# Optimization experiments

Measured on AMD Instinct MI355X. Metric: run time of the kernel, lower is better.

Reference implementation:

```python
import jax, jax.numpy as jnp
import numpy as np


def setup_inputs() -> dict:
    key = jax.random.key(0)
    ks = jax.random.split(key, 9)
    B, C, H, W = 4, 256, 64, 64
    Ci = C // 2
    s = 0.05  # keep activations numerically tame
    return {
        "x": jax.random.normal(ks[0], (B, C, H, W), jnp.float32),
        "w_g": jax.random.normal(ks[1], (Ci, C), jnp.float32) * s,
        "b_g": jax.random.normal(ks[2], (Ci,), jnp.float32) * s,
        "w_theta": jax.random.normal(ks[3], (Ci, C), jnp.float32) * s,
        "b_theta": jax.random.normal(ks[4], (Ci,), jnp.float32) * s,
        "w_phi": jax.random.normal(ks[5], (Ci, C), jnp.float32) * s,
        "b_phi": jax.random.normal(ks[6], (Ci,), jnp.float32) * s,
        "w_out": jax.random.normal(ks[7], (C, Ci), jnp.float32) * s,
        "b_out": jax.random.normal(ks[8], (C,), jnp.float32) * s,
    }


def reference(x, w_g, b_g, w_theta, b_theta, w_phi, b_phi, w_out, b_out):
    B, C, H, W = x.shape
    Ci = w_g.shape[0]
    N = H * W
    xr = x.reshape(B, C, N)  # flatten spatial dims

    def proj(w, b):  # 1x1 conv == per-pixel GEMM
        return jnp.einsum("oc,bcn->bon", w, xr) + b[None, :, None]

    g_x = proj(w_g, b_g)          # [B, Ci, N]
    theta_x = proj(w_theta, b_theta)
    phi_x = proj(w_phi, b_phi)

    scale = jnp.asarray(Ci, x.dtype) ** 0.5
    f = jnp.einsum("bci,bcj->bij", theta_x, phi_x) / scale  # [B, N, N]
    attn = jax.nn.softmax(f, axis=-1)

    # out[b,c,i] = sum_j g_x[b,c,j] * attn[b,i,j]
    out = jnp.einsum("bcj,bij->bci", g_x, attn)             # [B, Ci, N]
    y = jnp.einsum("oc,bcn->bon", w_out, out) + b_out[None, :, None]
    return y.reshape(B, C, H, W) + x
```

## Files before the change

kernel.cpp:

```cpp
#include <hip/hip_runtime.h>
#include <hip/hip_bf16.h>


typedef float f32x4 __attribute__((ext_vector_type(4)));
typedef float f32x16 __attribute__((ext_vector_type(16)));
typedef short s16x8 __attribute__((ext_vector_type(8)));
typedef short s16x4 __attribute__((ext_vector_type(4)));

#define B_  4
#define C_  256
#define CI_ 128
#define N_  4096

#define OFF_Q    (8ull  << 20)
#define OFF_K    (12ull << 20)
#define OFF_G    (16ull << 20)
#define OFF_WQK  (24ull << 20)
#define OFF_WG   (OFF_WQK + 131072)
#define OFF_WOUT (OFF_WG  + 65536)
#define OFF_BQK  (OFF_WOUT + 65536)
#define OFF_BG   (OFF_BQK + 1024)
#define OFF_BOUT (OFF_BG  + 512)
#define OFF_END  (OFF_BOUT + 1024)

__device__ inline f32x4 mfma16(s16x8 a, s16x8 b, f32x4 c) {
    return __builtin_amdgcn_mfma_f32_16x16x32_bf16(a, b, c, 0, 0, 0);
}
__device__ inline f32x16 mfma32(s16x8 a, s16x8 b, f32x16 c) {
    return __builtin_amdgcn_mfma_f32_32x32x16_bf16(a, b, c, 0, 0, 0);
}
__device__ inline s16x8 ld8(const __hip_bfloat16* p) { return *(const s16x8*)p; }
__device__ inline float b2f(short u) {
    return __uint_as_float(((unsigned int)(unsigned short)u) << 16);
}
__device__ inline unsigned int pk2(float a, float b) {
    __hip_bfloat162 h;
    h.x = __float2bfloat16(a); h.y = __float2bfloat16(b);
    return *(unsigned int*)&h;
}
__device__ inline void gload_lds16(const void* g, void* l) {
    __builtin_amdgcn_global_load_lds(
        (const __attribute__((address_space(1))) unsigned int*)g,
        (__attribute__((address_space(3))) unsigned int*)l, 16, 0, 0);
}
__device__ inline float fexp2(float x) { return __builtin_amdgcn_exp2f(x); }

__global__ void prep_weights(const float* wg, const float* bg,
                             const float* wt, const float* bt,
                             const float* wp, const float* bp,
                             const float* wo, const float* bo, char* ws) {
    __hip_bfloat16* Wqk  = (__hip_bfloat16*)(ws + OFF_WQK);
    __hip_bfloat16* Wg   = (__hip_bfloat16*)(ws + OFF_WG);
    __hip_bfloat16* Wout = (__hip_bfloat16*)(ws + OFF_WOUT);
    float* Bqk  = (float*)(ws + OFF_BQK);
    float* Bg   = (float*)(ws + OFF_BG);
    float* Bout = (float*)(ws + OFF_BOUT);
    const float rs = 0.08838834764831845f * 1.4426950408889634f;
    int idx = blockIdx.x * 256 + threadIdx.x;
    if (idx < 65536) {
        int r = idx >> 8, c = idx & 255;
        float v = (r < 128) ? wt[r * 256 + c] * rs : wp[(r - 128) * 256 + c];
        Wqk[idx] = __float2bfloat16(v);
    }
    if (idx < 32768) {
        Wg[idx]   = __float2bfloat16(wg[idx]);
        Wout[idx] = __float2bfloat16(wo[idx]);
    }
    if (idx < 256) { Bqk[idx] = (idx < 128) ? bt[idx] * rs : bp[idx - 128]; Bout[idx] = bo[idx]; }
    if (idx < 128) Bg[idx] = bg[idx];
}

__global__ __launch_bounds__(256) void proj(const float* x, char* ws) {
    const __hip_bfloat16* Wqk = (const __hip_bfloat16*)(ws + OFF_WQK);
    const __hip_bfloat16* Wg  = (const __hip_bfloat16*)(ws + OFF_WG);
    const float* Bqk = (const float*)(ws + OFF_BQK);
    const float* Bg  = (const float*)(ws + OFF_BG);
    __hip_bfloat16* Q  = (__hip_bfloat16*)(ws + OFF_Q);
    __hip_bfloat16* Kb = (__hip_bfloat16*)(ws + OFF_K);
    __hip_bfloat16* G  = (__hip_bfloat16*)(ws + OFF_G);

    __shared__ char at[32 * 512];

    int b = blockIdx.y, n0 = blockIdx.x * 32;
    int t = threadIdx.x;
    int w = t >> 6, l = t & 63, lr = l & 15, lg = l >> 4;

    {
        int n4 = (t & 7) * 4;
        int cp = t >> 3;
        const float* xb = x + ((size_t)b * C_) * N_ + n0 + n4;
#pragma unroll
        for (int p = 0; p < 4; p++) {
            int c0 = (p * 32 + cp) * 2;
            f32x4 vA = *(const f32x4*)(xb + (size_t)c0 * N_);
            f32x4 vB = *(const f32x4*)(xb + (size_t)(c0 + 1) * N_);
            int slot = c0 >> 3, coff = (c0 & 7) << 1;
#pragma unroll
            for (int i = 0; i < 4; i++) {
                int n = n4 + i;
                *(unsigned int*)(&at[n * 512 + ((slot ^ (n & 7)) << 4) + coff]) =
                    pk2(vA[i], vB[i]);
            }
        }
    }
    __syncthreads();

    f32x4 acc[4][2] = {};
    f32x4 accg[2][2] = {};
    int o0q = w * 64, o0g = w * 32;
#pragma unroll
    for (int kk = 0; kk < 8; kk++) {
        s16x8 a[2];
#pragma unroll
        for (int nf = 0; nf < 2; nf++) {
            int row = nf * 16 + lr;
            int s = (4 * kk + lg) ^ (row & 7);
            a[nf] = *(const s16x8*)(&at[row * 512 + s * 16]);
        }
#pragma unroll
        for (int of = 0; of < 4; of++) {
            s16x8 bb = ld8(Wqk + (size_t)(o0q + 16 * of + lr) * C_ + kk * 32 + lg * 8);
            acc[of][0] = mfma16(a[0], bb, acc[of][0]);
            acc[of][1] = mfma16(a[1], bb, acc[of][1]);
        }
#pragma unroll
        for (int og = 0; og < 2; og++) {
            s16x8 ag = ld8(Wg + (size_t)(o0g + 16 * og + lr) * C_ + kk * 32 + lg * 8);
            accg[og][0] = mfma16(ag, a[0], accg[og][0]);
            accg[og][1] = mfma16(ag, a[1], accg[og][1]);
        }
    }
#pragma unroll
    for (int of = 0; of < 4; of++) {
        int o = o0q + 16 * of + lr;
        float bias = Bqk[o];
#pragma unroll
        for (int nf = 0; nf < 2; nf++) {
#pragma unroll
            for (int i = 0; i < 4; i++) {
                int n = n0 + 16 * nf + lg * 4 + i;
                float v = acc[of][nf][i] + bias;
                if (o < 128) Q [(size_t)(b * N_ + n) * CI_ + o]         = __float2bfloat16(v);
                else         Kb[(size_t)(b * N_ + n) * CI_ + (o - 128)] = __float2bfloat16(v);
            }
        }
    }
#pragma unroll
    for (int og = 0; og < 2; og++) {
#pragma unroll
        for (int i = 0; i < 4; i++) {
            int o = o0g + 16 * og + lg * 4 + i;
            float bias = Bg[o];
#pragma unroll
            for (int nf = 0; nf < 2; nf++) {
                int n = n0 + 16 * nf + lr;
                G[(size_t)(b * CI_ + o) * N_ + n] = __float2bfloat16(accg[og][nf][i] + bias);
            }
        }
    }
}

__global__ __launch_bounds__(256, 3) void flash9(char* ws, int nchunk,
                                                 unsigned long long off_part,
                                                 unsigned long long off_ml) {
    const __hip_bfloat16* Q  = (const __hip_bfloat16*)(ws + OFF_Q);
    const __hip_bfloat16* Kb = (const __hip_bfloat16*)(ws + OFF_K);
    const __hip_bfloat16* G  = (const __hip_bfloat16*)(ws + OFF_G);
    __hip_bfloat16* OP = (__hip_bfloat16*)(ws + off_part);
    float* ML = (float*)(ws + off_ml);

    __shared__ char kbuf[2][32 * 256];
    __shared__ char vbuf[2][128 * 64];

    int L = blockIdx.x;
    int npairs = B_ * nchunk;
    int pair = L % npairs, qt = L / npairs;
    int b = pair / nchunk, cz = pair % nchunk;
    int per = 128 / nchunk, rem = 128 % nchunk;
    int jb_t = per * cz + (cz < rem ? cz : rem);
    int sz_t = per + (cz < rem ? 1 : 0);
    int jb = jb_t << 5, je = jb + (sz_t << 5);

    int w = threadIdx.x >> 6, l = threadIdx.x & 63;
    int cl = l & 31, hi = l >> 5;
    int q0 = qt * 128 + w * 32;
    int kkey = (l & 7) << 4;
    int vkey = (l >> 1) & 3;

    auto STAGE = [&](int pb_, int j0_) {
#pragma unroll
        for (int i = 0; i < 2; i++) {
            int row = w * 8 + i * 4 + (l >> 4);
            int bcol = ((l & 15) << 4) ^ ((row & 7) << 4);
            const char* src = (const char*)Kb + (((size_t)b * N_ + j0_ + row) << 8) + bcol;
            gload_lds16(src, &kbuf[pb_][(w * 8 + i * 4) * 256]);
        }
#pragma unroll
        for (int i = 0; i < 2; i++) {
            int c = w * 32 + i * 16 + (l >> 2);
            int srcslot = (l & 3) ^ ((l >> 3) & 3);
            const char* src = (const char*)G + ((((size_t)b * CI_ + c) * N_ + j0_) << 1)
                              + (srcslot << 4);
            gload_lds16(src, &vbuf[pb_][(w * 32 + i * 16) * 64]);
        }
    };

    s16x8 qb[8];
    {
        const __hip_bfloat16* qrow = Q + ((size_t)b * N_ + q0 + cl) * CI_ + hi * 8;
#pragma unroll
        for (int st = 0; st < 8; st++) qb[st] = ld8(qrow + st * 16);
    }

    f32x16 oacc[4] = {};
    float m_i = 0.f, lsum = 0.f;

    STAGE(0, jb);
    __syncthreads();
    int pb = 0;

    for (int j0 = jb; j0 < je; j0 += 32) {
        if (j0 + 32 < je) STAGE(pb ^ 1, j0 + 32);
        const char* kb = kbuf[pb];
        const char* vbb = vbuf[pb];
        f32x16 s = {};
        __builtin_amdgcn_s_setprio(1);
#pragma unroll
        for (int st = 0; st < 8; st++) {
            s16x8 kf = *(const s16x8*)(kb + cl * 256 + ((((st << 1) + hi) << 4) ^ kkey));
            s = mfma32(kf, qb[st], s);
        }
        __builtin_amdgcn_s_setprio(0);
        if (j0 == jb) {
            float t0 = fmaxf(fmaxf(s[0], s[1]), fmaxf(s[2], s[3]));
            float t1 = fmaxf(fmaxf(s[4], s[5]), fmaxf(s[6], s[7]));
            float t2 = fmaxf(fmaxf(s[8], s[9]), fmaxf(s[10], s[11]));
            float t3 = fmaxf(fmaxf(s[12], s[13]), fmaxf(s[14], s[15]));
            float tm = fmaxf(fmaxf(t0, t1), fmaxf(t2, t3));
            tm = fmaxf(tm, __shfl_xor(tm, 32));
            m_i = tm;
        }
#pragma unroll
        for (int r = 0; r < 16; r++) s[r] = fexp2(s[r] - m_i);
        lsum += ((s[0] + s[1]) + (s[2] + s[3])) + ((s[4] + s[5]) + (s[6] + s[7]))
              + ((s[8] + s[9]) + (s[10] + s[11])) + ((s[12] + s[13]) + (s[14] + s[15]));
        union { unsigned int u[4]; s16x8 v; } pa0, pa1;
#pragma unroll
        for (int i = 0; i < 4; i++) {
            pa0.u[i] = pk2(s[2 * i], s[2 * i + 1]);
            pa1.u[i] = pk2(s[8 + 2 * i], s[9 + 2 * i]);
        }
        __builtin_amdgcn_s_setprio(1);
#pragma unroll
        for (int u = 0; u < 2; u++) {
            s16x8 pa = u ? pa1.v : pa0.v;
#pragma unroll
            for (int cb = 0; cb < 4; cb++) {
                const char* base = vbb + ((cb * 32 + cl) << 6) + hi * 8;
                union { s16x4 h[2]; s16x8 v; } vf;
                vf.h[0] = *(const s16x4*)(base + ((((u << 1))     ^ vkey) << 4));
                vf.h[1] = *(const s16x4*)(base + ((((u << 1) | 1) ^ vkey) << 4));
                oacc[cb] = mfma32(pa, vf.v, oacc[cb]);
            }
        }
        __builtin_amdgcn_s_setprio(0);
        __syncthreads();
        pb ^= 1;
    }
    lsum += __shfl_xor(lsum, 32);
#pragma unroll
    for (int cb = 0; cb < 4; cb++) {
#pragma unroll
        for (int r = 0; r < 16; r++) {
            int q = q0 + (r & 3) + 8 * (r >> 2) + 4 * hi;
            OP[((size_t)(cz * B_ + b) * N_ + q) * CI_ + cb * 32 + cl] =
                __float2bfloat16(oacc[cb][r]);
        }
    }
    if (l < 32) {
        size_t mi = ((size_t)(cz * B_ + b) * N_ + q0 + l) * 2;
        ML[mi] = m_i;
        ML[mi + 1] = lsum;
    }
}

template <int NC>
__global__ __launch_bounds__(256) void out_fused2(const float* x, char* ws, float* y,
                                                  unsigned long long off_part,
                                                  unsigned long long off_ml) {
    const __hip_bfloat16* OP = (const __hip_bfloat16*)(ws + off_part);
    const float* ML = (const float*)(ws + off_ml);
    const __hip_bfloat16* Wo = (const __hip_bfloat16*)(ws + OFF_WOUT);
    const float* Bout = (const float*)(ws + OFF_BOUT);

    __shared__ char oT[16 * 256];

    int b = blockIdx.y;
    int n0 = blockIdx.x * 16;
    int t = threadIdx.x;

    {
        int nl = t >> 4;
        int cg = t & 15;
        int n = n0 + nl;
        float mz[NC], lz[NC], M = -1e30f;
#pragma unroll
        for (int z = 0; z < NC; z++) {
            size_t mi = ((size_t)(z * B_ + b) * N_ + n) * 2;
            mz[z] = ML[mi]; lz[z] = ML[mi + 1];
            M = fmaxf(M, mz[z]);
        }
        float Ls = 0.f, wz[NC];
#pragma unroll
        for (int z = 0; z < NC; z++) { wz[z] = fexp2(mz[z] - M); Ls += lz[z] * wz[z]; }
        float inv = 1.f / Ls;
        float o8[8] = {};
#pragma unroll
        for (int z = 0; z < NC; z++) {
            s16x8 v = ld8(OP + ((size_t)(z * B_ + b) * N_ + n) * CI_ + cg * 8);
            float wv = wz[z] * inv;
#pragma unroll
            for (int e = 0; e < 8; e++) o8[e] += wv * b2f(v[e]);
        }
        union { unsigned int u[4]; s16x8 v; } r;
#pragma unroll
        for (int e = 0; e < 4; e++) r.u[e] = pk2(o8[2 * e], o8[2 * e + 1]);
        *(s16x8*)(&oT[nl * 256 + ((cg ^ (nl & 7)) << 4)]) = r.v;
    }
    __syncthreads();

    int w = t >> 6, l = t & 63, lr = l & 15, lg = l >> 4;
    int o0 = w * 64;
    f32x4 acc[4] = {};
#pragma unroll
    for (int kk = 0; kk < 4; kk++) {
        int slot = kk * 4 + lg;
        s16x8 bb = *(const s16x8*)(&oT[lr * 256 + ((slot ^ (lr & 7)) << 4)]);
#pragma unroll
        for (int of = 0; of < 4; of++) {
            s16x8 a = ld8(Wo + (size_t)(o0 + 16 * of + lr) * CI_ + kk * 32 + lg * 8);
            acc[of] = mfma16(a, bb, acc[of]);
        }
    }
#pragma unroll
    for (int of = 0; of < 4; of++) {
#pragma unroll
        for (int i = 0; i < 4; i++) {
            int o = o0 + 16 * of + lg * 4 + i;
            int n = n0 + lr;
            size_t idx = (size_t)(b * C_ + o) * N_ + n;
            y[idx] = acc[of][i] + Bout[o] + x[idx];
        }
    }
}

extern "C" void kernel_launch(void* const* d_in, const int* in_sizes, int n_in,
                              void* d_out, int out_size, void* d_ws, size_t ws_size,
                              hipStream_t stream) {
    const float* x  = (const float*)d_in[0];
    const float* wg = (const float*)d_in[1];
    const float* bg = (const float*)d_in[2];
    const float* wt = (const float*)d_in[3];
    const float* bt = (const float*)d_in[4];
    const float* wp = (const float*)d_in[5];
    const float* bp = (const float*)d_in[6];
    const float* wo = (const float*)d_in[7];
    const float* bo = (const float*)d_in[8];
    char* ws = (char*)d_ws;
    float* y = (float*)d_out;

    unsigned long long need6 = OFF_END + (24ull << 20) + (1ull << 20);
    unsigned long long need4 = OFF_END + (16ull << 20) + (1ull << 20);
    int nchunk;
    unsigned long long off_part, off_ml;
    if (ws_size >= need6) {
        nchunk = 6; off_part = OFF_END; off_ml = OFF_END + (24ull << 20);
    } else if (ws_size >= need4) {
        nchunk = 4; off_part = OFF_END; off_ml = OFF_END + (16ull << 20);
    } else {
        nchunk = 2; off_part = 0ull; off_ml = OFF_END;
    }

    prep_weights<<<256, 256, 0, stream>>>(wg, bg, wt, bt, wp, bp, wo, bo, ws);
    proj<<<dim3(128, 4), 256, 0, stream>>>(x, ws);
    flash9<<<dim3(32 * B_ * nchunk), 256, 0, stream>>>(ws, nchunk, off_part, off_ml);
    if (nchunk == 6)
        out_fused2<6><<<dim3(256, 4), 256, 0, stream>>>(x, ws, y, off_part, off_ml);
    else if (nchunk == 4)
        out_fused2<4><<<dim3(256, 4), 256, 0, stream>>>(x, ws, y, off_part, off_ml);
    else
        out_fused2<2><<<dim3(256, 4), 256, 0, stream>>>(x, ws, y, off_part, off_ml);
}
```

Baseline: 95.92 us.

## Rewrite flash attention kernel with 16x16 MFMA tiles and LDS-staged P

The attention kernel moves from 32x32x16 MFMAs with 128-query blocks to 16x16x32 MFMAs with 64-query blocks, where each wave handles 16 queries. P is re-laid out through a small per-wave LDS buffer before the PV product. Occupancy is raised to 4 blocks per CU and the 6-chunk key split is dropped in favour of at most 4 chunks. More blocks and higher occupancy trade against twice the K/V staging per query and the extra LDS round-trip for P.

```diff
diff --git a/kernel.cpp b/kernel.cpp
--- a/kernel.cpp
+++ b/kernel.cpp
@@ -3,9 +3,7 @@
 
 
 typedef float f32x4 __attribute__((ext_vector_type(4)));
-typedef float f32x16 __attribute__((ext_vector_type(16)));
 typedef short s16x8 __attribute__((ext_vector_type(8)));
-typedef short s16x4 __attribute__((ext_vector_type(4)));
 
 #define B_  4
 #define C_  256
@@ -25,9 +23,6 @@
 
 __device__ inline f32x4 mfma16(s16x8 a, s16x8 b, f32x4 c) {
     return __builtin_amdgcn_mfma_f32_16x16x32_bf16(a, b, c, 0, 0, 0);
-}
-__device__ inline f32x16 mfma32(s16x8 a, s16x8 b, f32x16 c) {
-    return __builtin_amdgcn_mfma_f32_32x32x16_bf16(a, b, c, 0, 0, 0);
 }
 __device__ inline s16x8 ld8(const __hip_bfloat16* p) { return *(const s16x8*)p; }
 __device__ inline float b2f(short u) {
@@ -160,9 +155,9 @@
     }
 }
 
-__global__ __launch_bounds__(256, 3) void flash9(char* ws, int nchunk,
-                                                 unsigned long long off_part,
-                                                 unsigned long long off_ml) {
+__global__ __launch_bounds__(256, 4) void flash16(char* ws, int nchunk,
+                                                  unsigned long long off_part,
+                                                  unsigned long long off_ml) {
     const __hip_bfloat16* Q  = (const __hip_bfloat16*)(ws + OFF_Q);
     const __hip_bfloat16* Kb = (const __hip_bfloat16*)(ws + OFF_K);
     const __hip_bfloat16* G  = (const __hip_bfloat16*)(ws + OFF_G);
@@ -171,21 +166,20 @@
 
     __shared__ char kbuf[2][32 * 256];
     __shared__ char vbuf[2][128 * 64];
+    __shared__ char pbuf[4][1024];
 
     int L = blockIdx.x;
     int npairs = B_ * nchunk;
     int pair = L % npairs, qt = L / npairs;
     int b = pair / nchunk, cz = pair % nchunk;
-    int per = 128 / nchunk, rem = 128 % nchunk;
-    int jb_t = per * cz + (cz < rem ? cz : rem);
-    int sz_t = per + (cz < rem ? 1 : 0);
-    int jb = jb_t << 5, je = jb + (sz_t << 5);
-
-    int w = threadIdx.x >> 6, l = threadIdx.x & 63;
-    int cl = l & 31, hi = l >> 5;
-    int q0 = qt * 128 + w * 32;
-    int kkey = (l & 7) << 4;
-    int vkey = (l >> 1) & 3;
+    int CH = N_ / nchunk;
+    int jb = cz * CH, je = jb + CH;
+
+    int w = threadIdx.x >> 6, l = threadIdx.x & 63, lr = l & 15, lg = l >> 4;
+    int q0 = qt * 64 + w * 16;
+    int swz  = (lr & 7) << 4;
+    int pswz = ((lr >> 1) & 3) << 4;
+    char* pw = &pbuf[w][0];
 
     auto STAGE = [&](int pb_, int j0_) {
 #pragma unroll
@@ -205,14 +199,14 @@
         }
     };
 
-    s16x8 qb[8];
+    s16x8 qa[4];
     {
-        const __hip_bfloat16* qrow = Q + ((size_t)b * N_ + q0 + cl) * CI_ + hi * 8;
-#pragma unroll
-        for (int st = 0; st < 8; st++) qb[st] = ld8(qrow + st * 16);
-    }
-
-    f32x16 oacc[4] = {};
+        const __hip_bfloat16* qrow = Q + ((size_t)b * N_ + q0 + lr) * CI_ + lg * 8;
+#pragma unroll
+        for (int kk = 0; kk < 4; kk++) qa[kk] = ld8(qrow + kk * 32);
+    }
+
+    f32x4 oacc[8] = {};
     float m_i = 0.f, lsum = 0.f;
 
     STAGE(0, jb);
@@ -223,62 +217,69 @@
         if (j0 + 32 < je) STAGE(pb ^ 1, j0 + 32);
         const char* kb = kbuf[pb];
         const char* vbb = vbuf[pb];
-        f32x16 s = {};
+        f32x4 s[2] = {};
         __builtin_amdgcn_s_setprio(1);
 #pragma unroll
-        for (int st = 0; st < 8; st++) {
-            s16x8 kf = *(const s16x8*)(kb + cl * 256 + ((((st << 1) + hi) << 4) ^ kkey));
-            s = mfma32(kf, qb[st], s);
+        for (int kk = 0; kk < 4; kk++) {
+            int bc = ((kk << 6) + (lg << 4)) ^ swz;
+            s16x8 kf0 = *(const s16x8*)(kb + lr * 256 + bc);
+            s16x8 kf1 = *(const s16x8*)(kb + (16 + lr) * 256 + bc);
+            s[0] = mfma16(kf0, qa[kk], s[0]);
+            s[1] = mfma16(kf1, qa[kk], s[1]);
         }
         __builtin_amdgcn_s_setprio(0);
         if (j0 == jb) {
-            float t0 = fmaxf(fmaxf(s[0], s[1]), fmaxf(s[2], s[3]));
-            float t1 = fmaxf(fmaxf(s[4], s[5]), fmaxf(s[6], s[7]));
-            float t2 = fmaxf(fmaxf(s[8], s[9]), fmaxf(s[10], s[11]));
-            float t3 = fmaxf(fmaxf(s[12], s[13]), fmaxf(s[14], s[15]));
-            float tm = fmaxf(fmaxf(t0, t1), fmaxf(t2, t3));
+            f32x4 m4;
+            m4[0] = fmaxf(s[0][0], s[1][0]); m4[1] = fmaxf(s[0][1], s[1][1]);
+            m4[2] = fmaxf(s[0][2], s[1][2]); m4[3] = fmaxf(s[0][3], s[1][3]);
+            float tm = fmaxf(fmaxf(m4[0], m4[1]), fmaxf(m4[2], m4[3]));
+            tm = fmaxf(tm, __shfl_xor(tm, 16));
             tm = fmaxf(tm, __shfl_xor(tm, 32));
             m_i = tm;
         }
-#pragma unroll
-        for (int r = 0; r < 16; r++) s[r] = fexp2(s[r] - m_i);
-        lsum += ((s[0] + s[1]) + (s[2] + s[3])) + ((s[4] + s[5]) + (s[6] + s[7]))
-              + ((s[8] + s[9]) + (s[10] + s[11])) + ((s[12] + s[13]) + (s[14] + s[15]));
-        union { unsigned int u[4]; s16x8 v; } pa0, pa1;
-#pragma unroll
-        for (int i = 0; i < 4; i++) {
-            pa0.u[i] = pk2(s[2 * i], s[2 * i + 1]);
-            pa1.u[i] = pk2(s[8 + 2 * i], s[9 + 2 * i]);
-        }
+        {
+            f32x4 sum4 = {};
+#pragma unroll
+            for (int t = 0; t < 2; t++) {
+#pragma unroll
+                for (int i = 0; i < 4; i++) s[t][i] = fexp2(s[t][i] - m_i);
+                sum4 += s[t];
+            }
+            lsum += (sum4[0] + sum4[1]) + (sum4[2] + sum4[3]);
+            char* base = pw + lr * 64;
+#pragma unroll
+            for (int t = 0; t < 2; t++) {
+                unsigned int lo = pk2(s[t][0], s[t][1]);
+                unsigned int hi = pk2(s[t][2], s[t][3]);
+                int slot = t * 2 + (lg >> 1);
+                int byte0 = ((slot << 4) ^ pswz) + ((lg & 1) << 3);
+                *(unsigned int*)(base + byte0)     = lo;
+                *(unsigned int*)(base + byte0 + 4) = hi;
+            }
+        }
+        s16x8 pa = *(const s16x8*)(pw + lr * 64 + ((lg << 4) ^ pswz));
         __builtin_amdgcn_s_setprio(1);
 #pragma unroll
-        for (int u = 0; u < 2; u++) {
-            s16x8 pa = u ? pa1.v : pa0.v;
-#pragma unroll
-            for (int cb = 0; cb < 4; cb++) {
-                const char* base = vbb + ((cb * 32 + cl) << 6) + hi * 8;
-                union { s16x4 h[2]; s16x8 v; } vf;
-                vf.h[0] = *(const s16x4*)(base + ((((u << 1))     ^ vkey) << 4));
-                vf.h[1] = *(const s16x4*)(base + ((((u << 1) | 1) ^ vkey) << 4));
-                oacc[cb] = mfma32(pa, vf.v, oacc[cb]);
-            }
+        for (int cf = 0; cf < 8; cf++) {
+            s16x8 vb = *(const s16x8*)(vbb + ((16 * cf + lr) << 6) +
+                                       ((lg << 4) ^ pswz));
+            oacc[cf] = mfma16(pa, vb, oacc[cf]);
         }
         __builtin_amdgcn_s_setprio(0);
         __syncthreads();
         pb ^= 1;
     }
+    lsum += __shfl_xor(lsum, 16);
     lsum += __shfl_xor(lsum, 32);
 #pragma unroll
-    for (int cb = 0; cb < 4; cb++) {
-#pragma unroll
-        for (int r = 0; r < 16; r++) {
-            int q = q0 + (r & 3) + 8 * (r >> 2) + 4 * hi;
-            OP[((size_t)(cz * B_ + b) * N_ + q) * CI_ + cb * 32 + cl] =
-                __float2bfloat16(oacc[cb][r]);
-        }
-    }
-    if (l < 32) {
-        size_t mi = ((size_t)(cz * B_ + b) * N_ + q0 + l) * 2;
+    for (int i = 0; i < 4; i++) {
+        size_t row = ((size_t)(cz * B_ + b) * N_ + q0 + lg * 4 + i) * CI_;
+#pragma unroll
+        for (int cf = 0; cf < 8; cf++)
+            OP[row + 16 * cf + lr] = __float2bfloat16(oacc[cf][i]);
+    }
+    if (lg == 0) {
+        size_t mi = ((size_t)(cz * B_ + b) * N_ + q0 + lr) * 2;
         ML[mi] = m_i;
         ML[mi + 1] = lsum;
     }
@@ -369,13 +370,10 @@
     char* ws = (char*)d_ws;
     float* y = (float*)d_out;
 
-    unsigned long long need6 = OFF_END + (24ull << 20) + (1ull << 20);
     unsigned long long need4 = OFF_END + (16ull << 20) + (1ull << 20);
     int nchunk;
     unsigned long long off_part, off_ml;
-    if (ws_size >= need6) {
-        nchunk = 6; off_part = OFF_END; off_ml = OFF_END + (24ull << 20);
-    } else if (ws_size >= need4) {
+    if (ws_size >= need4) {
         nchunk = 4; off_part = OFF_END; off_ml = OFF_END + (16ull << 20);
     } else {
         nchunk = 2; off_part = 0ull; off_ml = OFF_END;
@@ -383,10 +381,8 @@
 
     prep_weights<<<256, 256, 0, stream>>>(wg, bg, wt, bt, wp, bp, wo, bo, ws);
     proj<<<dim3(128, 4), 256, 0, stream>>>(x, ws);
-    flash9<<<dim3(32 * B_ * nchunk), 256, 0, stream>>>(ws, nchunk, off_part, off_ml);
-    if (nchunk == 6)
-        out_fused2<6><<<dim3(256, 4), 256, 0, stream>>>(x, ws, y, off_part, off_ml);
-    else if (nchunk == 4)
+    flash16<<<dim3(64 * B_ * nchunk), 256, 0, stream>>>(ws, nchunk, off_part, off_ml);
+    if (nchunk == 4)
         out_fused2<4><<<dim3(256, 4), 256, 0, stream>>>(x, ws, y, off_part, off_ml);
     else
         out_fused2<2><<<dim3(256, 4), 256, 0, stream>>>(x, ws, y, off_part, off_ml);
```

Result: slower. 99.50 us (+3.7%).
